# Optimization experiments

Measured on AMD Instinct MI355X. Metric: run time of the kernel, lower is better.

The kernel has to match this reference:

```python
import jax, jax.numpy as jnp
import numpy as np

SIGMA = 45.0
N, M, D = 4096, 4096, 1024


def setup_inputs() -> dict:
    key = jax.random.key(0)
    k1, k2 = jax.random.split(key)
    inputs = jax.random.normal(k1, (N, D), dtype=jnp.float32)
    samples = jax.random.normal(k2, (M, D), dtype=jnp.float32)
    return {"inputs": inputs, "samples": samples}


def _sq_dists(x, y):
    # ||x_i||^2 + ||y_j||^2 - 2 x_i.y_j  -> [N, M]
    prod = x @ y.T
    xs = jnp.sum(x * x, axis=1)[:, None]
    ys = jnp.sum(y * y, axis=1)[None, :]
    return xs + ys - 2.0 * prod


def reference(inputs, samples):
    n = inputs.shape[0]
    m = samples.shape[0]
    x = inputs.reshape(n, -1)
    y = samples.reshape(m, -1)
    inv_s2 = 1.0 / (SIGMA ** 2)

    k_xx = _sq_dists(x, x)
    k_yy = _sq_dists(y, y)
    k_xy = _sq_dists(x, y)

    # unbiased MMD: exclude diagonal terms of k_xx, k_yy
    exx = jnp.exp(-k_xx * inv_s2)
    eyy = jnp.exp(-k_yy * inv_s2)
    exy = jnp.exp(-k_xy * inv_s2)

    mmd = (jnp.sum(exx) - jnp.sum(jnp.exp(-jnp.diag(k_xx) * inv_s2))) / (n * (n - 1))
    mmd = mmd + (jnp.sum(eyy) - jnp.sum(jnp.exp(-jnp.diag(k_yy) * inv_s2))) / (m * (m - 1))
    mmd = mmd - 2.0 / (n * m) * jnp.sum(exy)
    return mmd
```

## Files before the change

kernel.cpp:

```cpp
#include <hip/hip_runtime.h>
#include <math.h>


typedef _Float16 f16_t;
typedef _Float16 f16x4 __attribute__((ext_vector_type(4)));
typedef _Float16 f16x8 __attribute__((ext_vector_type(8)));
typedef float floatx4 __attribute__((ext_vector_type(4)));

#define NROWS 4096
#define MROWS 4096
#define DDIM  1024
#define BM    128
#define BK    32
#define NT    (NROWS / BM)
#define TRI   (NT * (NT + 1) / 2)
#define NBLK  (2 * TRI + NT * NT)

__global__ __launch_bounds__(256) void convert_kernel(
    const float* __restrict__ X, const float* __restrict__ Y,
    f16_t* __restrict__ Xh, f16_t* __restrict__ Yh,
    float* __restrict__ nx, float* __restrict__ ny) {
    const int wid  = threadIdx.x >> 6;
    const int lane = threadIdx.x & 63;
    const int row  = blockIdx.x * 4 + wid;
    const float* src;
    f16_t* dst;
    float* nrm;
    int r;
    if (row < NROWS) {
        r = row;         src = X + (size_t)r * DDIM;
        dst = Xh + (size_t)r * DDIM;  nrm = nx;
    } else {
        r = row - NROWS; src = Y + (size_t)r * DDIM;
        dst = Yh + (size_t)r * DDIM;  nrm = ny;
    }
    const float4* s4 = (const float4*)src;
    f16x4* d4 = (f16x4*)dst;
    float s = 0.f;
    #pragma unroll
    for (int c = 0; c < 4; c++) {
        float4 v = s4[c * 64 + lane];
        f16x4 h;
        h[0] = (f16_t)v.x; h[1] = (f16_t)v.y;
        h[2] = (f16_t)v.z; h[3] = (f16_t)v.w;
        d4[c * 64 + lane] = h;
        float h0 = (float)h[0], h1 = (float)h[1];
        float h2 = (float)h[2], h3 = (float)h[3];
        s += h0 * h0 + h1 * h1 + h2 * h2 + h3 * h3;
    }
    #pragma unroll
    for (int off = 32; off > 0; off >>= 1) s += __shfl_down(s, off);
    if (lane == 0) nrm[r] = s;
}

__global__ __launch_bounds__(256) void mmd_mfma(
    const f16_t* __restrict__ Xh, const f16_t* __restrict__ Yh,
    const float* __restrict__ nx, const float* __restrict__ ny,
    double* __restrict__ partials) {
    __shared__ __align__(16) f16_t lds[2 * BM * BK];
    __shared__ double wred[4];

    const int b = blockIdx.x;
    const f16_t *A, *B;
    const float *nA, *nB;
    int tr, tc;
    double coef;
    if (b < 2 * TRI) {
        int u = (b < TRI) ? b : b - TRI;
        int r = 0;
        while (u >= NT - r) { u -= NT - r; r++; }
        tr = r; tc = r + u;
        double w = (tr == tc) ? 1.0 : 2.0;
        if (b < TRI) { A = Xh; B = Xh; nA = nx; nB = nx;
                       coef = w / ((double)NROWS * (double)(NROWS - 1)); }
        else         { A = Yh; B = Yh; nA = ny; nB = ny;
                       coef = w / ((double)MROWS * (double)(MROWS - 1)); }
    } else {
        int u = b - 2 * TRI;
        tr = u / NT; tc = u % NT;
        A = Xh; B = Yh; nA = nx; nB = ny;
        coef = -2.0 / ((double)NROWS * (double)MROWS);
    }

    const int t    = threadIdx.x;
    const int wave = t >> 6;
    const int lane = t & 63;
    const int wm   = wave >> 1;
    const int wn   = wave & 1;

    const f16_t* Abase = A + (size_t)tr * BM * DDIM;
    const f16_t* Bbase = B + (size_t)tc * BM * DDIM;
    const int lrow = lane >> 2;
    const int lcol = (lane & 3) * 8;
    const f16_t* gsrc[4];
    f16_t* gdst[4];
    #pragma unroll
    for (int i = 0; i < 4; i++) {
        int idx = wave * 4 + i;
        int tile = idx >> 3;
        int rg   = idx & 7;
        const f16_t* base = tile ? Bbase : Abase;
        gsrc[i] = base + (size_t)(rg * 16 + lrow) * DDIM + lcol;
        gdst[i] = lds + tile * BM * BK + (rg * 16 + lrow) * BK + lcol;
    }

    const int m    = lane & 15;
    const int quad = lane >> 4;

    float na[16], nb[4];
    #pragma unroll
    for (int i = 0; i < 4; i++) {
        #pragma unroll
        for (int r = 0; r < 4; r++)
            na[i * 4 + r] = nA[tr * BM + wm * 64 + i * 16 + quad * 4 + r];
        nb[i] = nB[tc * BM + wn * 64 + i * 16 + m];
    }

    floatx4 acc_r[4][4];
    #pragma unroll
    for (int i = 0; i < 4; i++)
        #pragma unroll
        for (int j = 0; j < 4; j++) acc_r[i][j] = (floatx4){0.f, 0.f, 0.f, 0.f};

    for (int k0 = 0; k0 < DDIM; k0 += BK) {
        __syncthreads();
        #pragma unroll
        for (int i = 0; i < 4; i++) {
            __builtin_amdgcn_global_load_lds(
                (const __attribute__((address_space(1))) void*)(gsrc[i] + k0),
                (__attribute__((address_space(3))) void*)gdst[i],
                16, 0, 0);
        }
        __syncthreads();

        f16x8 ah[4], bh[4];
        #pragma unroll
        for (int s = 0; s < 4; s++) {
            int arow = wm * 64 + s * 16 + m;
            int brow = wn * 64 + s * 16 + m;
            ah[s] = *(const f16x8*)&lds[(0 * BM + arow) * BK + quad * 8];
            bh[s] = *(const f16x8*)&lds[(1 * BM + brow) * BK + quad * 8];
        }
        #pragma unroll
        for (int i = 0; i < 4; i++)
            #pragma unroll
            for (int j = 0; j < 4; j++)
                acc_r[i][j] = __builtin_amdgcn_mfma_f32_16x16x32_f16(ah[i], bh[j], acc_r[i][j], 0, 0, 0);
    }

    const float inv_s2 = 1.0f / 2025.0f;
    float lsum = 0.f;
    #pragma unroll
    for (int i = 0; i < 4; i++)
        #pragma unroll
        for (int j = 0; j < 4; j++)
            #pragma unroll
            for (int r = 0; r < 4; r++) {
                float arg = (2.f * acc_r[i][j][r] - na[i * 4 + r] - nb[j]) * inv_s2;
                lsum += __expf(arg);
            }

    double d = (double)lsum;
    #pragma unroll
    for (int off = 32; off > 0; off >>= 1) d += __shfl_down(d, off);
    if (lane == 0) wred[wave] = d;
    __syncthreads();
    if (t == 0)
        partials[b] = (wred[0] + wred[1] + wred[2] + wred[3]) * coef;
}

__global__ __launch_bounds__(256) void final_reduce(const double* __restrict__ partials,
                                                    float* __restrict__ out) {
    __shared__ double red[256];
    int t = threadIdx.x;
    double s = 0.0;
    for (int i = t; i < NBLK; i += 256) s += partials[i];
    red[t] = s;
    __syncthreads();
    for (int off = 128; off > 0; off >>= 1) {
        if (t < off) red[t] += red[t + off];
        __syncthreads();
    }
    if (t == 0) {
        double mmd = red[0] - 1.0 / (double)(NROWS - 1) - 1.0 / (double)(MROWS - 1);
        out[0] = (float)mmd;
    }
}

extern "C" void kernel_launch(void* const* d_in, const int* in_sizes, int n_in,
                              void* d_out, int out_size, void* d_ws, size_t ws_size,
                              hipStream_t stream) {
    const float* X = (const float*)d_in[0];
    const float* Y = (const float*)d_in[1];
    float* out = (float*)d_out;

    char* p = (char*)d_ws;
    double* partials = (double*)p;            p += ((size_t)NBLK * sizeof(double) + 255) & ~255ULL;
    float* nx = (float*)p;                    p += (size_t)NROWS * sizeof(float);
    float* ny = (float*)p;                    p += (size_t)MROWS * sizeof(float);
    f16_t* Xh = (f16_t*)p;                    p += (size_t)NROWS * DDIM * sizeof(f16_t);
    f16_t* Yh = (f16_t*)p;

    convert_kernel<<<(NROWS + MROWS) / 4, 256, 0, stream>>>(X, Y, Xh, Yh, nx, ny);
    mmd_mfma<<<NBLK, 256, 0, stream>>>(Xh, Yh, nx, ny, partials);
    final_reduce<<<1, 256, 0, stream>>>(partials, out);
}
```

Before: 164.9 us.

## Load MFMA operands directly from global into registers with double buffering

Removes the LDS staging and the two per-iteration barriers. Each wave now loads its A/B fragments straight from global memory into registers, using a two-stage register prefetch over 64-wide K steps, and a launch-bounds occupancy hint is added. This drops the sync overhead, but operand reuse across waves through shared memory is lost, so each wave fetches its own rows and global/L2 traffic roughly doubles, with narrow 16-byte strided loads.

```diff
diff --git a/kernel.cpp b/kernel.cpp
--- a/kernel.cpp
+++ b/kernel.cpp
@@ -11,7 +11,6 @@
 #define MROWS 4096
 #define DDIM  1024
 #define BM    128
-#define BK    32
 #define NT    (NROWS / BM)
 #define TRI   (NT * (NT + 1) / 2)
 #define NBLK  (2 * TRI + NT * NT)
@@ -53,11 +52,10 @@
     if (lane == 0) nrm[r] = s;
 }
 
-__global__ __launch_bounds__(256) void mmd_mfma(
+__global__ __launch_bounds__(256, 3) void mmd_mfma(
     const f16_t* __restrict__ Xh, const f16_t* __restrict__ Yh,
     const float* __restrict__ nx, const float* __restrict__ ny,
     double* __restrict__ partials) {
-    __shared__ __align__(16) f16_t lds[2 * BM * BK];
     __shared__ double wred[4];
 
     const int b = blockIdx.x;
@@ -87,25 +85,53 @@
     const int lane = t & 63;
     const int wm   = wave >> 1;
     const int wn   = wave & 1;
-
-    const f16_t* Abase = A + (size_t)tr * BM * DDIM;
-    const f16_t* Bbase = B + (size_t)tc * BM * DDIM;
-    const int lrow = lane >> 2;
-    const int lcol = (lane & 3) * 8;
-    const f16_t* gsrc[4];
-    f16_t* gdst[4];
-    #pragma unroll
-    for (int i = 0; i < 4; i++) {
-        int idx = wave * 4 + i;
-        int tile = idx >> 3;
-        int rg   = idx & 7;
-        const f16_t* base = tile ? Bbase : Abase;
-        gsrc[i] = base + (size_t)(rg * 16 + lrow) * DDIM + lcol;
-        gdst[i] = lds + tile * BM * BK + (rg * 16 + lrow) * BK + lcol;
-    }
-
     const int m    = lane & 15;
     const int quad = lane >> 4;
+
+    const f16_t* arow[4];
+    const f16_t* brow[4];
+    #pragma unroll
+    for (int s = 0; s < 4; s++) {
+        arow[s] = A + (size_t)(tr * BM + wm * 64 + s * 16 + m) * DDIM + quad * 8;
+        brow[s] = B + (size_t)(tc * BM + wn * 64 + s * 16 + m) * DDIM + quad * 8;
+    }
+
+    floatx4 acc[4][4];
+    #pragma unroll
+    for (int i = 0; i < 4; i++)
+        #pragma unroll
+        for (int j = 0; j < 4; j++) acc[i][j] = (floatx4){0.f, 0.f, 0.f, 0.f};
+
+    f16x8 a0[4], b0[4], a1[4], b1[4];
+    #pragma unroll
+    for (int s = 0; s < 4; s++) {
+        a0[s] = *(const f16x8*)(arow[s]);
+        b0[s] = *(const f16x8*)(brow[s]);
+    }
+    for (int k0 = 0; k0 < DDIM; k0 += 64) {
+        #pragma unroll
+        for (int s = 0; s < 4; s++) {
+            a1[s] = *(const f16x8*)(arow[s] + k0 + 32);
+            b1[s] = *(const f16x8*)(brow[s] + k0 + 32);
+        }
+        #pragma unroll
+        for (int i = 0; i < 4; i++)
+            #pragma unroll
+            for (int j = 0; j < 4; j++)
+                acc[i][j] = __builtin_amdgcn_mfma_f32_16x16x32_f16(a0[i], b0[j], acc[i][j], 0, 0, 0);
+        if (k0 + 64 < DDIM) {
+            #pragma unroll
+            for (int s = 0; s < 4; s++) {
+                a0[s] = *(const f16x8*)(arow[s] + k0 + 64);
+                b0[s] = *(const f16x8*)(brow[s] + k0 + 64);
+            }
+        }
+        #pragma unroll
+        for (int i = 0; i < 4; i++)
+            #pragma unroll
+            for (int j = 0; j < 4; j++)
+                acc[i][j] = __builtin_amdgcn_mfma_f32_16x16x32_f16(a1[i], b1[j], acc[i][j], 0, 0, 0);
+    }
 
     float na[16], nb[4];
     #pragma unroll
@@ -115,39 +141,6 @@
             na[i * 4 + r] = nA[tr * BM + wm * 64 + i * 16 + quad * 4 + r];
         nb[i] = nB[tc * BM + wn * 64 + i * 16 + m];
     }
-
-    floatx4 acc_r[4][4];
-    #pragma unroll
-    for (int i = 0; i < 4; i++)
-        #pragma unroll
-        for (int j = 0; j < 4; j++) acc_r[i][j] = (floatx4){0.f, 0.f, 0.f, 0.f};
-
-    for (int k0 = 0; k0 < DDIM; k0 += BK) {
-        __syncthreads();
-        #pragma unroll
-        for (int i = 0; i < 4; i++) {
-            __builtin_amdgcn_global_load_lds(
-                (const __attribute__((address_space(1))) void*)(gsrc[i] + k0),
-                (__attribute__((address_space(3))) void*)gdst[i],
-                16, 0, 0);
-        }
-        __syncthreads();
-
-        f16x8 ah[4], bh[4];
-        #pragma unroll
-        for (int s = 0; s < 4; s++) {
-            int arow = wm * 64 + s * 16 + m;
-            int brow = wn * 64 + s * 16 + m;
-            ah[s] = *(const f16x8*)&lds[(0 * BM + arow) * BK + quad * 8];
-            bh[s] = *(const f16x8*)&lds[(1 * BM + brow) * BK + quad * 8];
-        }
-        #pragma unroll
-        for (int i = 0; i < 4; i++)
-            #pragma unroll
-            for (int j = 0; j < 4; j++)
-                acc_r[i][j] = __builtin_amdgcn_mfma_f32_16x16x32_f16(ah[i], bh[j], acc_r[i][j], 0, 0, 0);
-    }
-
     const float inv_s2 = 1.0f / 2025.0f;
     float lsum = 0.f;
     #pragma unroll
@@ -156,7 +149,7 @@
         for (int j = 0; j < 4; j++)
             #pragma unroll
             for (int r = 0; r < 4; r++) {
-                float arg = (2.f * acc_r[i][j][r] - na[i * 4 + r] - nb[j]) * inv_s2;
+                float arg = (2.f * acc[i][j][r] - na[i * 4 + r] - nb[j]) * inv_s2;
                 lsum += __expf(arg);
             }
 
```

New measurement: 337.7 us. +104.7%, slower.

## Enlarge MFMA block tile to 256x256 with 8 waves per block

Applied to the files above, without the earlier changes.

Doubles the output tile per block from 128x128 to 256x256 and runs 512 threads (8 waves) per block. Each wave now computes a 64x128 sub-tile with 32 accumulators, which gives more MFMA work per LDS fragment load and halves the global traffic per output element. In exchange it uses more registers and LDS per block and launches fewer blocks: the grid is about a quarter of its former size, which may leave some CUs idle or cause load imbalance. Diagonal tiles of the symmetric XX and YY parts also waste a larger share of their work.

```diff
diff --git a/kernel.cpp b/kernel.cpp
--- a/kernel.cpp
+++ b/kernel.cpp
@@ -10,8 +10,9 @@
 #define NROWS 4096
 #define MROWS 4096
 #define DDIM  1024
-#define BM    128
+#define BM    256
 #define BK    32
+#define TILE  (BM * BK)
 #define NT    (NROWS / BM)
 #define TRI   (NT * (NT + 1) / 2)
 #define NBLK  (2 * TRI + NT * NT)
@@ -53,12 +54,12 @@
     if (lane == 0) nrm[r] = s;
 }
 
-__global__ __launch_bounds__(256) void mmd_mfma(
+__global__ __launch_bounds__(512, 2) void mmd_mfma(
     const f16_t* __restrict__ Xh, const f16_t* __restrict__ Yh,
     const float* __restrict__ nx, const float* __restrict__ ny,
     double* __restrict__ partials) {
-    __shared__ __align__(16) f16_t lds[2 * BM * BK];
-    __shared__ double wred[4];
+    __shared__ __align__(16) f16_t lds[2 * TILE];
+    __shared__ double wred[8];
 
     const int b = blockIdx.x;
     const f16_t *A, *B;
@@ -93,34 +94,35 @@
     const int lrow = lane >> 2;
     const int lcol = (lane & 3) * 8;
     const f16_t* gsrc[4];
-    f16_t* gdst[4];
+    int ldsoff[4];
     #pragma unroll
     for (int i = 0; i < 4; i++) {
         int idx = wave * 4 + i;
-        int tile = idx >> 3;
-        int rg   = idx & 7;
+        int tile = idx >> 4;
+        int rg   = idx & 15;
         const f16_t* base = tile ? Bbase : Abase;
         gsrc[i] = base + (size_t)(rg * 16 + lrow) * DDIM + lcol;
-        gdst[i] = lds + tile * BM * BK + (rg * 16 + lrow) * BK + lcol;
+        ldsoff[i] = tile * TILE + (rg * 16 + lrow) * BK + lcol;
     }
 
     const int m    = lane & 15;
     const int quad = lane >> 4;
 
-    float na[16], nb[4];
-    #pragma unroll
-    for (int i = 0; i < 4; i++) {
+    float na[16], nb[8];
+    #pragma unroll
+    for (int i = 0; i < 4; i++)
         #pragma unroll
         for (int r = 0; r < 4; r++)
             na[i * 4 + r] = nA[tr * BM + wm * 64 + i * 16 + quad * 4 + r];
-        nb[i] = nB[tc * BM + wn * 64 + i * 16 + m];
-    }
-
-    floatx4 acc_r[4][4];
+    #pragma unroll
+    for (int j = 0; j < 8; j++)
+        nb[j] = nB[tc * BM + wn * 128 + j * 16 + m];
+
+    floatx4 acc[4][8];
     #pragma unroll
     for (int i = 0; i < 4; i++)
         #pragma unroll
-        for (int j = 0; j < 4; j++) acc_r[i][j] = (floatx4){0.f, 0.f, 0.f, 0.f};
+        for (int j = 0; j < 8; j++) acc[i][j] = (floatx4){0.f, 0.f, 0.f, 0.f};
 
     for (int k0 = 0; k0 < DDIM; k0 += BK) {
         __syncthreads();
@@ -128,24 +130,27 @@
         for (int i = 0; i < 4; i++) {
             __builtin_amdgcn_global_load_lds(
                 (const __attribute__((address_space(1))) void*)(gsrc[i] + k0),
-                (__attribute__((address_space(3))) void*)gdst[i],
+                (__attribute__((address_space(3))) void*)(lds + ldsoff[i]),
                 16, 0, 0);
         }
         __syncthreads();
 
-        f16x8 ah[4], bh[4];
+        f16x8 ah[4], bh[8];
         #pragma unroll
         for (int s = 0; s < 4; s++) {
             int arow = wm * 64 + s * 16 + m;
-            int brow = wn * 64 + s * 16 + m;
-            ah[s] = *(const f16x8*)&lds[(0 * BM + arow) * BK + quad * 8];
-            bh[s] = *(const f16x8*)&lds[(1 * BM + brow) * BK + quad * 8];
+            ah[s] = *(const f16x8*)&lds[arow * BK + quad * 8];
+        }
+        #pragma unroll
+        for (int u = 0; u < 8; u++) {
+            int brow = wn * 128 + u * 16 + m;
+            bh[u] = *(const f16x8*)&lds[TILE + brow * BK + quad * 8];
         }
         #pragma unroll
         for (int i = 0; i < 4; i++)
             #pragma unroll
-            for (int j = 0; j < 4; j++)
-                acc_r[i][j] = __builtin_amdgcn_mfma_f32_16x16x32_f16(ah[i], bh[j], acc_r[i][j], 0, 0, 0);
+            for (int j = 0; j < 8; j++)
+                acc[i][j] = __builtin_amdgcn_mfma_f32_16x16x32_f16(ah[i], bh[j], acc[i][j], 0, 0, 0);
     }
 
     const float inv_s2 = 1.0f / 2025.0f;
@@ -153,10 +158,10 @@
     #pragma unroll
     for (int i = 0; i < 4; i++)
         #pragma unroll
-        for (int j = 0; j < 4; j++)
+        for (int j = 0; j < 8; j++)
             #pragma unroll
             for (int r = 0; r < 4; r++) {
-                float arg = (2.f * acc_r[i][j][r] - na[i * 4 + r] - nb[j]) * inv_s2;
+                float arg = (2.f * acc[i][j][r] - na[i * 4 + r] - nb[j]) * inv_s2;
                 lsum += __expf(arg);
             }
 
@@ -165,8 +170,12 @@
     for (int off = 32; off > 0; off >>= 1) d += __shfl_down(d, off);
     if (lane == 0) wred[wave] = d;
     __syncthreads();
-    if (t == 0)
-        partials[b] = (wred[0] + wred[1] + wred[2] + wred[3]) * coef;
+    if (t == 0) {
+        double s = 0.0;
+        #pragma unroll
+        for (int w = 0; w < 8; w++) s += wred[w];
+        partials[b] = s * coef;
+    }
 }
 
 __global__ __launch_bounds__(256) void final_reduce(const double* __restrict__ partials,
@@ -202,6 +211,6 @@
     f16_t* Yh = (f16_t*)p;
 
     convert_kernel<<<(NROWS + MROWS) / 4, 256, 0, stream>>>(X, Y, Xh, Yh, nx, ny);
-    mmd_mfma<<<NBLK, 256, 0, stream>>>(Xh, Yh, nx, ny, partials);
+    mmd_mfma<<<NBLK, 512, 0, stream>>>(Xh, Yh, nx, ny, partials);
     final_reduce<<<1, 256, 0, stream>>>(partials, out);
 }
```

New measurement: 195.3 us. +18.4%, slower.
